# Kernel tuning notes

Hardware: AMD Instinct MI355X
Metric: run time of the kernel (lower is better)

## Reference

```python
import jax, jax.numpy as jnp
import numpy as np
from jax import lax

B, C, H, W, K = 32, 128, 56, 56, 5
CR = C // 4          # reduced channels in weight-gen MLP
CE = 4 * C           # expanded channels
EPS = 1e-6


def setup_inputs() -> dict:
    key = jax.random.key(0)
    ks = jax.random.split(key, 8)
    s = lambda fan: 1.0 / np.sqrt(fan)
    return {
        "x": jax.random.normal(ks[0], (B, C, H, W), jnp.float32),
        "w_fc1": jax.random.normal(ks[1], (CR, C), jnp.float32) * s(C),
        "ln1_w": jnp.ones((CR,), jnp.float32),
        "ln1_b": jnp.zeros((CR,), jnp.float32),
        "w_fc2": jax.random.normal(ks[2], (C * K * K, CR), jnp.float32) * s(CR),
        "ln2_w": jnp.ones((C,), jnp.float32),
        "ln2_b": jnp.zeros((C,), jnp.float32),
        "w_expand": jax.random.normal(ks[3], (CE, C), jnp.float32) * s(C),
        "w_shrink": jax.random.normal(ks[4], (C, CE), jnp.float32) * s(CE),
        "grn_gamma": jax.random.normal(ks[5], (CE,), jnp.float32) * 0.1,
        "grn_beta": jax.random.normal(ks[6], (CE,), jnp.float32) * 0.1,
    }


def _ln(v, w, b, axis):
    u = v.mean(axis, keepdims=True)
    s2 = jnp.square(v - u).mean(axis, keepdims=True)
    return (v - u) * lax.rsqrt(s2 + EPS) * w + b


def reference(x, w_fc1, ln1_w, ln1_b, w_fc2, ln2_w, ln2_b, w_expand, w_shrink,
              grn_gamma, grn_beta):
    b, c, h, w = x.shape
    # ---- dynamic weight generation: pool -> fc1 -> LN -> fc2 ----
    pooled = x.mean((2, 3))                                  # [B, C]
    hdn = pooled @ w_fc1.T                                   # [B, CR]
    hdn = _ln(hdn, ln1_w, ln1_b, axis=-1)                    # channels_first LN over CR
    dyn = hdn @ w_fc2.T                                      # [B, C*K*K]
    dyn_w = dyn.reshape(b * c, 1, K, K)                      # per-sample depthwise kernels
    # ---- per-sample dynamic depthwise conv (groups = B*C) ----
    pad = K // 2
    out = lax.conv_general_dilated(
        x.reshape(1, b * c, h, w), dyn_w,
        window_strides=(1, 1), padding=[(pad, pad), (pad, pad)],
        dimension_numbers=("NCHW", "OIHW", "NCHW"),
        feature_group_count=b * c,
    ).reshape(b, c, h, w)
    # ---- LN (channels_first) over channel dim ----
    u = out.mean(1, keepdims=True)
    s2 = jnp.square(out - u).mean(1, keepdims=True)
    out = (out - u) * lax.rsqrt(s2 + EPS)
    out = ln2_w[None, :, None, None] * out + ln2_b[None, :, None, None]
    # ---- expand 1x1 -> GELU -> GRN -> shrink 1x1 ----
    out = jnp.einsum("bchw,oc->bohw", out, w_expand)         # [B, 4C, H, W]
    out = jax.nn.gelu(out, approximate=False)
    gx = jnp.sqrt(jnp.sum(jnp.square(out), axis=(2, 3), keepdims=True))  # [B,4C,1,1]
    nx = gx / (gx.mean(1, keepdims=True) + EPS)
    g = grn_gamma[None, :, None, None]
    bt = grn_beta[None, :, None, None]
    out = g * (out * nx) + bt + out
    out = jnp.einsum("bohw,co->bchw", out, w_shrink)         # [B, C, H, W]
    return out + x
```

## Files before the change

kernel.cpp:

```cpp
#include <hip/hip_runtime.h>
#include <hip/hip_bf16.h>

#define B_   32
#define C_   128
#define H_   56
#define W_   56
#define HW_  (H_*W_)
#define BHW_ (B_*HW_)
#define K5_  5
#define KK_  25
#define CR_  32
#define CE_  512
#define EPS_ 1e-6f

typedef __hip_bfloat16 bf16;
typedef __attribute__((ext_vector_type(8))) short short8;
typedef __attribute__((ext_vector_type(4))) float f32x4;


__device__ __forceinline__ float wave_reduce_sum(float v) {
#pragma unroll
  for (int off = 32; off > 0; off >>= 1) v += __shfl_down(v, off, 64);
  return v;
}
__device__ __forceinline__ float bf2f(unsigned short u) {
  return __uint_as_float(((unsigned)u) << 16);
}
__device__ __forceinline__ unsigned short f2bf_bits(float f) {
  bf16 h = __float2bfloat16(f);
  unsigned short u;
  __builtin_memcpy(&u, &h, 2);
  return u;
}
__device__ __forceinline__ float fast_gelu(float v) {
  float u = 0.7978845608f * v * (1.0f + 0.044715f * v * v);
  float a = fabsf(u);
  float t = __expf(-2.0f * a);
  float th = __builtin_copysignf((1.0f - t) / (1.0f + t), u);
  return 0.5f * v * (1.0f + th);
}

__global__ __launch_bounds__(256) void prep_kernel(const float* __restrict__ we,
                                                   const float* __restrict__ ws,
                                                   bf16* __restrict__ weB,
                                                   bf16* __restrict__ wsB) {
  int i = blockIdx.x * 256 + threadIdx.x;
  if (i < CE_ * C_) {
    weB[i] = __float2bfloat16(we[i]);
    wsB[i] = __float2bfloat16(ws[i]);
  }
}

__global__ __launch_bounds__(256) void pool_kernel(const float* __restrict__ x,
                                                   float* __restrict__ pooled) {
  int bc = blockIdx.x;
  const float* xp = x + (size_t)bc * HW_;
  float s = 0.f;
  for (int i = threadIdx.x; i < HW_; i += 256) s += xp[i];
  s = wave_reduce_sum(s);
  __shared__ float red[4];
  int lane = threadIdx.x & 63, wid = threadIdx.x >> 6;
  if (lane == 0) red[wid] = s;
  __syncthreads();
  if (threadIdx.x == 0) pooled[bc] = (red[0] + red[1] + red[2] + red[3]) * (1.0f / HW_);
}

__global__ __launch_bounds__(256) void fc_kernel(const float* __restrict__ pooled,
                                                 const float* __restrict__ w_fc1,
                                                 const float* __restrict__ ln1_w,
                                                 const float* __restrict__ ln1_b,
                                                 const float* __restrict__ w_fc2,
                                                 float* __restrict__ dyn) {
  int b = blockIdx.x;
  int tid = threadIdx.x;
  __shared__ float sp[C_];
  __shared__ float sh[CR_];
  __shared__ float shn[CR_];
  __shared__ float stats[2];
  if (tid < C_) sp[tid] = pooled[b * C_ + tid];
  __syncthreads();
  if (tid < CR_) {
    float acc = 0.f;
    const float* wr = w_fc1 + tid * C_;
#pragma unroll 4
    for (int c = 0; c < C_; ++c) acc += sp[c] * wr[c];
    sh[tid] = acc;
  }
  __syncthreads();
  if (tid == 0) {
    float u = 0.f;
    for (int j = 0; j < CR_; ++j) u += sh[j];
    u *= (1.0f / CR_);
    float v = 0.f;
    for (int j = 0; j < CR_; ++j) { float d = sh[j] - u; v += d * d; }
    v *= (1.0f / CR_);
    stats[0] = u;
    stats[1] = rsqrtf(v + EPS_);
  }
  __syncthreads();
  if (tid < CR_) shn[tid] = (sh[tid] - stats[0]) * stats[1] * ln1_w[tid] + ln1_b[tid];
  __syncthreads();
  for (int i = tid; i < C_ * KK_; i += 256) {
    const float* wr = w_fc2 + i * CR_;
    float acc = 0.f;
#pragma unroll
    for (int j = 0; j < CR_; ++j) acc += shn[j] * wr[j];
    dyn[b * (C_ * KK_) + i] = acc;
  }
}

__global__ __launch_bounds__(256) void conv_kernel(const float* __restrict__ x,
                                                   const float* __restrict__ dyn,
                                                   bf16* __restrict__ z) {
  int bc = blockIdx.x;
  int b = bc >> 7;
  int c = bc & 127;
  int tid = threadIdx.x;
  __shared__ float xs[H_ * 64];
  __shared__ float wks[KK_];
  if (tid < H_ * 4) {
    int r = tid >> 2, q = tid & 3;
    int col = (q < 2) ? q : (56 + q);
    xs[r * 64 + col] = 0.f;
  }
  if (tid < KK_) wks[tid] = dyn[b * (C_ * KK_) + c * KK_ + tid];
  const float4* xp4 = reinterpret_cast<const float4*>(x + (size_t)bc * HW_);
  for (int i = tid; i < 784; i += 256) {
    float4 v = xp4[i];
    int h = i / 14, w4 = (i % 14) * 4;
    float* dst = &xs[h * 64 + 2 + w4];
    dst[0] = v.x; dst[1] = v.y; dst[2] = v.z; dst[3] = v.w;
  }
  __syncthreads();
  float wr[KK_];
#pragma unroll
  for (int j = 0; j < KK_; ++j) wr[j] = wks[j];
  for (int g = tid; g < 784; g += 256) {
    int h = g / 14;
    int w4 = (g % 14) * 4;
    float a0 = 0.f, a1 = 0.f, a2 = 0.f, a3 = 0.f;
#pragma unroll
    for (int dh = 0; dh < K5_; ++dh) {
      int hh = h + dh - 2;
      if (hh < 0 || hh >= H_) continue;
      const float* row = &xs[hh * 64 + w4];
      float4 va = *reinterpret_cast<const float4*>(row);
      float4 vb = *reinterpret_cast<const float4*>(row + 4);
      float v0 = va.x, v1 = va.y, v2 = va.z, v3 = va.w;
      float v4 = vb.x, v5 = vb.y, v6 = vb.z, v7 = vb.w;
      float u0 = wr[dh * 5 + 0], u1 = wr[dh * 5 + 1], u2 = wr[dh * 5 + 2];
      float u3 = wr[dh * 5 + 3], u4 = wr[dh * 5 + 4];
      a0 += v0 * u0 + v1 * u1 + v2 * u2 + v3 * u3 + v4 * u4;
      a1 += v1 * u0 + v2 * u1 + v3 * u2 + v4 * u3 + v5 * u4;
      a2 += v2 * u0 + v3 * u1 + v4 * u2 + v5 * u3 + v6 * u4;
      a3 += v3 * u0 + v4 * u1 + v5 * u2 + v6 * u3 + v7 * u4;
    }
    size_t base = (size_t)bc * HW_ + h * W_ + w4;
    ushort4 pk = make_ushort4(f2bf_bits(a0), f2bf_bits(a1), f2bf_bits(a2), f2bf_bits(a3));
    *reinterpret_cast<ushort4*>(reinterpret_cast<unsigned short*>(z) + base) = pk;
  }
}

__global__ __launch_bounds__(256) void ln_kernel(const bf16* __restrict__ z,
                                                 const float* __restrict__ ln2_w,
                                                 const float* __restrict__ ln2_b,
                                                 bf16* __restrict__ yT) {
  int hw0 = blockIdx.x * 64;
  int b = blockIdx.y;
  int tid = threadIdx.x;
  int wq = tid & 63;
  int cq = tid >> 6;
  __shared__ unsigned short zt[C_][64];
  __shared__ float redS[4][64];
  __shared__ float redQ[4][64];
  __shared__ float meanArr[64];
  __shared__ float invArr[64];
  float s = 0.f, q = 0.f;
  const unsigned short* zp = reinterpret_cast<const unsigned short*>(z);
#pragma unroll 4
  for (int k = 0; k < 32; ++k) {
    int c = cq * 32 + k;
    unsigned short u = zp[((size_t)(b * C_ + c)) * HW_ + hw0 + wq];
    float v = bf2f(u);
    s += v;
    q += v * v;
    zt[c][wq] = u;
  }
  redS[cq][wq] = s;
  redQ[cq][wq] = q;
  __syncthreads();
  if (cq == 0) {
    float ss = redS[0][wq] + redS[1][wq] + redS[2][wq] + redS[3][wq];
    float qq = redQ[0][wq] + redQ[1][wq] + redQ[2][wq] + redQ[3][wq];
    float m = ss * (1.0f / C_);
    float var = qq * (1.0f / C_) - m * m;
    meanArr[wq] = m;
    invArr[wq] = rsqrtf(fmaxf(var, 0.f) + EPS_);
  }
  __syncthreads();
  float m = meanArr[wq], iv = invArr[wq];
  unsigned short* yp =
      reinterpret_cast<unsigned short*>(yT) + ((size_t)(b * HW_ + hw0 + wq)) * C_ + cq * 32;
#pragma unroll
  for (int g = 0; g < 4; ++g) {
    unsigned short pk[8];
#pragma unroll
    for (int i = 0; i < 8; ++i) {
      int c = cq * 32 + g * 8 + i;
      float v = bf2f(zt[c][wq]);
      pk[i] = f2bf_bits((v - m) * iv * ln2_w[c] + ln2_b[c]);
    }
    int4 t;
    __builtin_memcpy(&t, pk, 16);
    *reinterpret_cast<int4*>(yp + g * 8) = t;
  }
}

__global__ __launch_bounds__(256) void expand_mfma(const bf16* __restrict__ yT,
                                                   const bf16* __restrict__ weB,
                                                   bf16* __restrict__ eT,
                                                   float* __restrict__ gx2) {
  int j0 = blockIdx.x * 128;
  int o0 = blockIdx.y * 128;
  int tid = threadIdx.x;
  int lane = tid & 63, wid = tid >> 6;
  int wm = wid >> 1, wn = wid & 1;
  int quad = lane >> 4, l15 = lane & 15;
  __shared__ short As[128][40];
  __shared__ short Bs[128][40];
  f32x4 acc[4][4] = {};
  const short* yTs = reinterpret_cast<const short*>(yT);
  const short* weS = reinterpret_cast<const short*>(weB);
  for (int k0 = 0; k0 < C_; k0 += 32) {
#pragma unroll
    for (int t = tid; t < 512; t += 256) {
      int r = t >> 2, ch = t & 3;
      int4 va = *reinterpret_cast<const int4*>(yTs + (size_t)(j0 + r) * C_ + k0 + ch * 8);
      *reinterpret_cast<int4*>(&As[r][ch * 8]) = va;
      int4 vb = *reinterpret_cast<const int4*>(weS + (size_t)(o0 + r) * C_ + k0 + ch * 8);
      *reinterpret_cast<int4*>(&Bs[r][ch * 8]) = vb;
    }
    __syncthreads();
    short8 a[4], bfr[4];
#pragma unroll
    for (int mf = 0; mf < 4; ++mf)
      a[mf] = *reinterpret_cast<const short8*>(&As[wm * 64 + mf * 16 + l15][quad * 8]);
#pragma unroll
    for (int nf = 0; nf < 4; ++nf)
      bfr[nf] = *reinterpret_cast<const short8*>(&Bs[wn * 64 + nf * 16 + l15][quad * 8]);
#pragma unroll
    for (int mf = 0; mf < 4; ++mf)
#pragma unroll
      for (int nf = 0; nf < 4; ++nf)
        acc[mf][nf] = __builtin_amdgcn_mfma_f32_16x16x32_bf16(a[mf], bfr[nf], acc[mf][nf], 0, 0, 0);
    __syncthreads();
  }
  unsigned short* eP = reinterpret_cast<unsigned short*>(eT);
#pragma unroll
  for (int mf = 0; mf < 4; ++mf) {
    int jm = j0 + wm * 64 + mf * 16;
    int bb = jm / HW_;
    int jb = jm + quad * 4;
#pragma unroll
    for (int nf = 0; nf < 4; ++nf) {
      int o = o0 + wn * 64 + nf * 16 + l15;
      float g2 = 0.f;
#pragma unroll
      for (int r = 0; r < 4; ++r) {
        float ge = fast_gelu(acc[mf][nf][r]);
        g2 += ge * ge;
        eP[(size_t)(jb + r) * CE_ + o] = f2bf_bits(ge);
      }
      g2 += __shfl_xor(g2, 16, 64);
      g2 += __shfl_xor(g2, 32, 64);
      if (quad == 0) atomicAdd(&gx2[bb * CE_ + o], g2);
    }
  }
}

__global__ __launch_bounds__(512) void grn_scale_kernel(const float* __restrict__ gx2,
                                                        const float* __restrict__ gamma,
                                                        float* __restrict__ scale) {
  int b = blockIdx.x;
  int o = threadIdx.x;
  float gx = sqrtf(gx2[b * CE_ + o]);
  float s = wave_reduce_sum(gx);
  __shared__ float red[8];
  __shared__ float meansh;
  int lane = o & 63, wid = o >> 6;
  if (lane == 0) red[wid] = s;
  __syncthreads();
  if (o == 0) {
    float t = 0.f;
    for (int i = 0; i < 8; ++i) t += red[i];
    meansh = t * (1.0f / CE_);
  }
  __syncthreads();
  scale[b * CE_ + o] = 1.0f + gamma[o] * (gx / (meansh + EPS_));
}

__global__ __launch_bounds__(128) void sb_kernel(const float* __restrict__ w_shrink,
                                                 const float* __restrict__ beta,
                                                 float* __restrict__ sb) {
  int c = threadIdx.x;
  float acc = 0.f;
  for (int o = 0; o < CE_; ++o) acc += w_shrink[c * CE_ + o] * beta[o];
  sb[c] = acc;
}

__global__ __launch_bounds__(256) void shrink_mfma(const bf16* __restrict__ eT,
                                                   const bf16* __restrict__ wsB,
                                                   const float* __restrict__ scale,
                                                   const float* __restrict__ sb,
                                                   const float* __restrict__ x,
                                                   float* __restrict__ out) {
  int j0 = blockIdx.x * 128;
  int tid = threadIdx.x;
  int lane = tid & 63, wid = tid >> 6;
  int wm = wid >> 1, wn = wid & 1;
  int quad = lane >> 4, l15 = lane & 15;
  __shared__ short As[128][40];
  __shared__ short Bs[128][40];
  f32x4 acc[4][4] = {};
  const short* eS = reinterpret_cast<const short*>(eT);
  const short* wsS = reinterpret_cast<const short*>(wsB);
  for (int k0 = 0; k0 < CE_; k0 += 32) {
#pragma unroll
    for (int t = tid; t < 512; t += 256) {
      int r = t >> 2, ch = t & 3;
      int jj = j0 + r;
      int bb = jj / HW_;
      union { int4 i4; unsigned short us[8]; } uv;
      uv.i4 = *reinterpret_cast<const int4*>(eS + (size_t)jj * CE_ + k0 + ch * 8);
      const float* sp = scale + bb * CE_ + k0 + ch * 8;
      unsigned short pk[8];
#pragma unroll
      for (int i = 0; i < 8; ++i) pk[i] = f2bf_bits(bf2f(uv.us[i]) * sp[i]);
      int4 t4;
      __builtin_memcpy(&t4, pk, 16);
      *reinterpret_cast<int4*>(&As[r][ch * 8]) = t4;
      int4 vb = *reinterpret_cast<const int4*>(wsS + (size_t)r * CE_ + k0 + ch * 8);
      *reinterpret_cast<int4*>(&Bs[r][ch * 8]) = vb;
    }
    __syncthreads();
    short8 a[4], bfr[4];
#pragma unroll
    for (int mf = 0; mf < 4; ++mf)
      a[mf] = *reinterpret_cast<const short8*>(&As[wm * 64 + mf * 16 + l15][quad * 8]);
#pragma unroll
    for (int nf = 0; nf < 4; ++nf)
      bfr[nf] = *reinterpret_cast<const short8*>(&Bs[wn * 64 + nf * 16 + l15][quad * 8]);
#pragma unroll
    for (int mf = 0; mf < 4; ++mf)
#pragma unroll
      for (int nf = 0; nf < 4; ++nf)
        acc[mf][nf] = __builtin_amdgcn_mfma_f32_16x16x32_bf16(a[mf], bfr[nf], acc[mf][nf], 0, 0, 0);
    __syncthreads();
  }
#pragma unroll
  for (int mf = 0; mf < 4; ++mf) {
    int jb = j0 + wm * 64 + mf * 16 + quad * 4;
    int bb = jb / HW_;
    int hw = jb - bb * HW_;
#pragma unroll
    for (int nf = 0; nf < 4; ++nf) {
      int c = wn * 64 + nf * 16 + l15;
      size_t base = ((size_t)(bb * C_ + c)) * HW_ + hw;
      float add = sb[c];
      float4 xv = *reinterpret_cast<const float4*>(x + base);
      float4 ov;
      ov.x = acc[mf][nf][0] + add + xv.x;
      ov.y = acc[mf][nf][1] + add + xv.y;
      ov.z = acc[mf][nf][2] + add + xv.z;
      ov.w = acc[mf][nf][3] + add + xv.w;
      *reinterpret_cast<float4*>(out + base) = ov;
    }
  }
}

extern "C" void kernel_launch(void* const* d_in, const int* in_sizes, int n_in,
                              void* d_out, int out_size, void* d_ws, size_t ws_size,
                              hipStream_t stream) {
  (void)in_sizes; (void)n_in; (void)out_size; (void)ws_size;
  const float* x        = (const float*)d_in[0];
  const float* w_fc1    = (const float*)d_in[1];
  const float* ln1_w    = (const float*)d_in[2];
  const float* ln1_b    = (const float*)d_in[3];
  const float* w_fc2    = (const float*)d_in[4];
  const float* ln2_w    = (const float*)d_in[5];
  const float* ln2_b    = (const float*)d_in[6];
  const float* w_expand = (const float*)d_in[7];
  const float* w_shrink = (const float*)d_in[8];
  const float* gamma    = (const float*)d_in[9];
  const float* beta     = (const float*)d_in[10];
  float* out = (float*)d_out;

  char* ws = (char*)d_ws;
  float* pooled = (float*)(ws + 0);
  float* dyn    = (float*)(ws + 16384);
  float* gx2    = (float*)(ws + 425984);
  float* scale  = (float*)(ws + 491520);
  float* sb     = (float*)(ws + 557056);
  bf16*  weB    = (bf16*)(ws + 557568);
  bf16*  wsB    = (bf16*)(ws + 688640);
  bf16*  yT     = (bf16*)(ws + 819712);
  bf16*  eT     = (bf16*)(ws + 26509824);
  bf16*  z      = eT;

  prep_kernel<<<256, 256, 0, stream>>>(w_expand, w_shrink, weB, wsB);
  pool_kernel<<<B_ * C_, 256, 0, stream>>>(x, pooled);
  fc_kernel<<<B_, 256, 0, stream>>>(pooled, w_fc1, ln1_w, ln1_b, w_fc2, dyn);
  conv_kernel<<<B_ * C_, 256, 0, stream>>>(x, dyn, z);
  ln_kernel<<<dim3(49, B_), 256, 0, stream>>>(z, ln2_w, ln2_b, yT);
  hipMemsetAsync(gx2, 0, B_ * CE_ * sizeof(float), stream);
  expand_mfma<<<dim3(784, 4), 256, 0, stream>>>(yT, weB, eT, gx2);
  grn_scale_kernel<<<B_, 512, 0, stream>>>(gx2, gamma, scale);
  sb_kernel<<<1, 128, 0, stream>>>(w_shrink, beta, sb);
  shrink_mfma<<<784, 256, 0, stream>>>(eT, wsB, scale, sb, x, out);
}
```

Before: 316.3 us.

## Fold GRN scale into per-batch shrink weights and use sigmoid GELU approximation

The per-sample GRN scale is no longer applied to every activation element inside the shrink GEMM's load loop. A new small kernel multiplies it into a per-batch bf16 copy of the shrink weights, and shrink_mfma is re-gridded per batch (25 spatial tiles by 32 batches), with clamped loads and skipped stores for the partial last tile. The tanh-based GELU is replaced with the cheaper x*sigmoid(1.702x) approximation, which trades extra numerical error for fewer ALU ops. Launch bounds now request 4 blocks per CU for both GEMM kernels.

```diff
diff --git a/kernel.cpp b/kernel.cpp
--- a/kernel.cpp
+++ b/kernel.cpp
@@ -33,11 +33,8 @@
   return u;
 }
 __device__ __forceinline__ float fast_gelu(float v) {
-  float u = 0.7978845608f * v * (1.0f + 0.044715f * v * v);
-  float a = fabsf(u);
-  float t = __expf(-2.0f * a);
-  float th = __builtin_copysignf((1.0f - t) / (1.0f + t), u);
-  return 0.5f * v * (1.0f + th);
+  float t = __expf(-1.702f * v);
+  return v * __builtin_amdgcn_rcpf(1.0f + t);
 }
 
 __global__ __launch_bounds__(256) void prep_kernel(const float* __restrict__ we,
@@ -216,10 +213,10 @@
   }
 }
 
-__global__ __launch_bounds__(256) void expand_mfma(const bf16* __restrict__ yT,
-                                                   const bf16* __restrict__ weB,
-                                                   bf16* __restrict__ eT,
-                                                   float* __restrict__ gx2) {
+__global__ __launch_bounds__(256, 4) void expand_mfma(const bf16* __restrict__ yT,
+                                                      const bf16* __restrict__ weB,
+                                                      bf16* __restrict__ eT,
+                                                      float* __restrict__ gx2) {
   int j0 = blockIdx.x * 128;
   int o0 = blockIdx.y * 128;
   int tid = threadIdx.x;
@@ -308,13 +305,25 @@
   sb[c] = acc;
 }
 
-__global__ __launch_bounds__(256) void shrink_mfma(const bf16* __restrict__ eT,
-                                                   const bf16* __restrict__ wsB,
-                                                   const float* __restrict__ scale,
-                                                   const float* __restrict__ sb,
-                                                   const float* __restrict__ x,
-                                                   float* __restrict__ out) {
-  int j0 = blockIdx.x * 128;
+__global__ __launch_bounds__(256) void scale_ws_kernel(const float* __restrict__ ws,
+                                                       const float* __restrict__ scale,
+                                                       bf16* __restrict__ sws) {
+  int c = blockIdx.x;
+  int b = blockIdx.y;
+  const float* sp = scale + b * CE_;
+  const float* wp = ws + (size_t)c * CE_;
+  bf16* op = sws + ((size_t)(b * C_ + c)) * CE_;
+  for (int i = threadIdx.x; i < CE_; i += 256)
+    op[i] = __float2bfloat16(wp[i] * sp[i]);
+}
+
+__global__ __launch_bounds__(256, 4) void shrink_mfma(const bf16* __restrict__ eT,
+                                                      const bf16* __restrict__ sws,
+                                                      const float* __restrict__ sb,
+                                                      const float* __restrict__ x,
+                                                      float* __restrict__ out) {
+  int hw0 = blockIdx.x * 128;
+  int b = blockIdx.y;
   int tid = threadIdx.x;
   int lane = tid & 63, wid = tid >> 6;
   int wm = wid >> 1, wn = wid & 1;
@@ -322,23 +331,15 @@
   __shared__ short As[128][40];
   __shared__ short Bs[128][40];
   f32x4 acc[4][4] = {};
-  const short* eS = reinterpret_cast<const short*>(eT);
-  const short* wsS = reinterpret_cast<const short*>(wsB);
+  const short* eS = reinterpret_cast<const short*>(eT) + (size_t)b * HW_ * CE_;
+  const short* wsS = reinterpret_cast<const short*>(sws) + (size_t)b * C_ * CE_;
   for (int k0 = 0; k0 < CE_; k0 += 32) {
 #pragma unroll
     for (int t = tid; t < 512; t += 256) {
       int r = t >> 2, ch = t & 3;
-      int jj = j0 + r;
-      int bb = jj / HW_;
-      union { int4 i4; unsigned short us[8]; } uv;
-      uv.i4 = *reinterpret_cast<const int4*>(eS + (size_t)jj * CE_ + k0 + ch * 8);
-      const float* sp = scale + bb * CE_ + k0 + ch * 8;
-      unsigned short pk[8];
-#pragma unroll
-      for (int i = 0; i < 8; ++i) pk[i] = f2bf_bits(bf2f(uv.us[i]) * sp[i]);
-      int4 t4;
-      __builtin_memcpy(&t4, pk, 16);
-      *reinterpret_cast<int4*>(&As[r][ch * 8]) = t4;
+      int hwc = hw0 + r; if (hwc >= HW_) hwc = HW_ - 1;
+      int4 va = *reinterpret_cast<const int4*>(eS + (size_t)hwc * CE_ + k0 + ch * 8);
+      *reinterpret_cast<int4*>(&As[r][ch * 8]) = va;
       int4 vb = *reinterpret_cast<const int4*>(wsS + (size_t)r * CE_ + k0 + ch * 8);
       *reinterpret_cast<int4*>(&Bs[r][ch * 8]) = vb;
     }
@@ -359,13 +360,12 @@
   }
 #pragma unroll
   for (int mf = 0; mf < 4; ++mf) {
-    int jb = j0 + wm * 64 + mf * 16 + quad * 4;
-    int bb = jb / HW_;
-    int hw = jb - bb * HW_;
+    int hw = hw0 + wm * 64 + mf * 16 + quad * 4;
+    if (hw >= HW_) continue;
 #pragma unroll
     for (int nf = 0; nf < 4; ++nf) {
       int c = wn * 64 + nf * 16 + l15;
-      size_t base = ((size_t)(bb * C_ + c)) * HW_ + hw;
+      size_t base = ((size_t)(b * C_ + c)) * HW_ + hw;
       float add = sb[c];
       float4 xv = *reinterpret_cast<const float4*>(x + base);
       float4 ov;
@@ -404,8 +404,10 @@
   bf16*  weB    = (bf16*)(ws + 557568);
   bf16*  wsB    = (bf16*)(ws + 688640);
   bf16*  yT     = (bf16*)(ws + 819712);
+  bf16*  sws    = (bf16*)(ws + 819712);
   bf16*  eT     = (bf16*)(ws + 26509824);
   bf16*  z      = eT;
+  (void)wsB;
 
   prep_kernel<<<256, 256, 0, stream>>>(w_expand, w_shrink, weB, wsB);
   pool_kernel<<<B_ * C_, 256, 0, stream>>>(x, pooled);
@@ -416,5 +418,6 @@
   expand_mfma<<<dim3(784, 4), 256, 0, stream>>>(yT, weB, eT, gx2);
   grn_scale_kernel<<<B_, 512, 0, stream>>>(gx2, gamma, scale);
   sb_kernel<<<1, 128, 0, stream>>>(w_shrink, beta, sb);
-  shrink_mfma<<<784, 256, 0, stream>>>(eT, wsB, scale, sb, x, out);
-}
+  scale_ws_kernel<<<dim3(C_, B_), 256, 0, stream>>>(w_shrink, scale, sws);
+  shrink_mfma<<<dim3(25, B_), 256, 0, stream>>>(eT, sws, sb, x, out);
+}
```

Result: faster. 303.0 us (-4.2%).
